# Performance work log

Hardware: AMD Instinct MI355X
Metric: run time of the kernel (lower is better)

Reference implementation:

```python
import jax, jax.numpy as jnp
import numpy as np

MAX_RADIUS = 4.0
N_BASIS = 10
MUL = 8                    # output_size -> '8x0e' multiplicity
OUT_MULS = (16, 8, 4)      # irreps_output = 16x0e + 8x1o + 4x2e
L_DIMS = (1, 3, 5)
N_NODES = 10000
N_EDGES = 131072
N_GRAPHS = 64
WEIGHT_NUMEL = MUL * MUL * sum(OUT_MULS)  # 1792


def _silu(x):
    return x * jax.nn.sigmoid(x)


def _sph_harm(u):
    # e3nn real spherical harmonics lmax=2, normalize=True, 'component' normalization
    x, y, z = u[:, 0], u[:, 1], u[:, 2]
    s3, s5, s15 = 3.0 ** 0.5, 5.0 ** 0.5, 15.0 ** 0.5
    sh0 = jnp.ones_like(x)[:, None]
    sh1 = jnp.stack([s3 * x, s3 * y, s3 * z], -1)
    sh2 = jnp.stack([s15 * x * z, s15 * x * y,
                     s5 * (y * y - 0.5 * (x * x + z * z)),
                     s15 * y * z, 0.5 * s15 * (z * z - x * x)], -1)
    return sh0, sh1, sh2


def _soft_one_hot(x):
    # e3nn soft_one_hot_linspace, basis='gaussian', cutoff=True
    values = jnp.linspace(0.0, MAX_RADIUS, N_BASIS + 2)[1:-1]
    step = MAX_RADIUS / (N_BASIS + 1)
    diff = (x[:, None] - values) / step
    return jnp.exp(-diff * diff) / 1.12


def setup_inputs() -> dict:
    key = jax.random.key(0)
    ks = jax.random.split(key, 16)
    return {
        "pos": jax.random.normal(ks[0], (N_NODES, 3), jnp.float32) * 2.0,
        "A": jax.random.randint(ks[1], (N_NODES,), 0, 10),
        "batch": jnp.sort(jax.random.randint(ks[2], (N_NODES,), 0, N_GRAPHS)),
        "edge_src": jax.random.randint(ks[3], (N_EDGES,), 0, N_NODES),
        "edge_dst": jax.random.randint(ks[4], (N_EDGES,), 0, N_NODES),
        "edge_shifts": jax.random.normal(ks[5], (N_EDGES, 3), jnp.float32) * 0.1,
        "cell": jax.random.normal(ks[6], (N_GRAPHS, 3, 3), jnp.float32),
        "embed_table": jax.random.normal(ks[7], (10, 16), jnp.float32),
        "fit_W1": jax.random.normal(ks[8], (16, 64), jnp.float32) * (2.0 / 16) ** 0.5,
        "fit_b1": jnp.zeros((64,), jnp.float32),
        "fit_W2": jax.random.normal(ks[9], (64, 32), jnp.float32) * (2.0 / 64) ** 0.5,
        "fit_b2": jnp.zeros((32,), jnp.float32),
        "fit_W3": jax.random.normal(ks[10], (32, MUL), jnp.float32) * (2.0 / 32) ** 0.5,
        "fit_b3": jnp.zeros((MUL,), jnp.float32),
        "fc_W1": jax.random.normal(ks[11], (N_BASIS, 64), jnp.float32),
        "fc_W2": jax.random.normal(ks[12], (64, 64), jnp.float32),
        "fc_W3": jax.random.normal(ks[13], (64, 64), jnp.float32),
        "fc_W4": jax.random.normal(ks[14], (64, WEIGHT_NUMEL), jnp.float32),
    }


def reference(pos, A, batch, edge_src, edge_dst, edge_shifts, cell,
              embed_table, fit_W1, fit_b1, fit_W2, fit_b2, fit_W3, fit_b3,
              fc_W1, fc_W2, fc_W3, fc_W4):
    # --- edge vectors with periodic shifts ---
    shift_vecs = jnp.einsum('ni,nij->nj', edge_shifts, cell[batch[edge_src]])
    edge_vec = pos[edge_dst] - pos[edge_src] + shift_vecs      # [E,3]
    edge_length = jnp.linalg.norm(edge_vec, axis=1)            # [E]
    unit = edge_vec / jnp.maximum(edge_length, 1e-9)[:, None]

    # --- per-node scalar features: embedding -> MLP (MainNet2) ---
    h = embed_table[A]
    h = _silu(h @ fit_W1 + fit_b1)
    h = _silu(h @ fit_W2 + fit_b2)
    Ai = h @ fit_W3 + fit_b3                                   # [N,8]

    sh0, sh1, sh2 = _sph_harm(unit)                            # [E,1],[E,3],[E,5]

    # --- radial MLP (e3nn FullyConnectedNet: silu, 1/sqrt(fan_in) weight scaling) ---
    emb = _soft_one_hot(edge_length) * (N_BASIS ** 0.5)
    w = _silu(emb @ fc_W1 / N_BASIS ** 0.5)
    w = _silu(w @ fc_W2 / 8.0)
    w = _silu(w @ fc_W3 / 8.0)
    w = w @ fc_W4 / 8.0                                        # [E,1792]

    Ai_src = Ai[edge_src]                                      # [E,8]
    Ai_dst = Ai[edge_dst]                                      # [E,8]

    # FullTensorProduct(8x0e, sh) is the outer product f_in[e,u,m] = Ai_src[e,u]*sh_l[e,m];
    # FullyConnectedTensorProduct with scalar irreps_in2 reduces per l-channel to a
    # weighted contraction with path normalization 1/sqrt(mul1*mul2) = 1/8.
    blocks, off = [], 0
    for mul_out, dim, sh_l in zip(OUT_MULS, L_DIMS, (sh0, sh1, sh2)):
        n = MUL * MUL * mul_out
        Wl = w[:, off:off + n].reshape(-1, MUL, MUL, mul_out)
        off += n
        blk = jnp.einsum('eu,em,ev,euvw->ewm', Ai_src, sh_l, Ai_dst, Wl) / MUL
        blocks.append(blk.reshape(-1, mul_out * dim))
    edge_features = jnp.concatenate(blocks, -1)                # [E,60]

    # --- scatter-mean aggregation to destination nodes ---
    n_nodes = pos.shape[0]
    counts = jax.ops.segment_sum(jnp.ones((edge_dst.shape[0],), jnp.float32),
                                 edge_dst, num_segments=n_nodes)
    out = jax.ops.segment_sum(edge_features, edge_dst, num_segments=n_nodes)
    return out / jnp.maximum(counts, 1.0)[:, None]             # [N,60]
```

## Files before the change

kernel.cpp:

```cpp
#include <hip/hip_runtime.h>
#include <hip/hip_bf16.h>
#include <math.h>

#define NN 10000
#define NE 131072

typedef __attribute__((ext_vector_type(8))) short short8;
typedef __attribute__((ext_vector_type(4))) float f32x4;

__device__ __forceinline__ float silu_f(float x) {
    return x / (1.0f + __expf(-x));
}

__device__ __forceinline__ unsigned short f2bf(float f) {
    unsigned int u = __float_as_uint(f);
    u += 0x7FFFu + ((u >> 16) & 1u);
    return (unsigned short)(u >> 16);
}

__device__ __forceinline__ unsigned int pk_bf16(float lo, float hi) {
    __hip_bfloat162 h = __float22bfloat162_rn(float2{lo, hi});
    return *reinterpret_cast<unsigned int*>(&h);
}

__global__ __launch_bounds__(256)
void prep_kernel(const int* __restrict__ A,
                 const int* __restrict__ edst,
                 const float* __restrict__ emb_tab,
                 const float* __restrict__ W1, const float* __restrict__ b1,
                 const float* __restrict__ W2, const float* __restrict__ b2,
                 const float* __restrict__ W3, const float* __restrict__ b3,
                 const float* __restrict__ fcW1,
                 const float* __restrict__ fcW2,
                 const float* __restrict__ fcW3,
                 const float* __restrict__ fcW4,
                 int* __restrict__ hist,
                 float* __restrict__ outg,
                 float* __restrict__ Ai,
                 unsigned short* __restrict__ Wg,
                 unsigned short* __restrict__ Bg)
{
    const int blk = blockIdx.x;
    const int tid = threadIdx.x;

    if (blk < 40) {
        int nd = blk * 256 + tid;
        if (nd >= NN) return;
        int a = A[nd];
        float h[16];
#pragma unroll
        for (int i = 0; i < 16; ++i) h[i] = emb_tab[a * 16 + i];
        float h1[64];
#pragma unroll
        for (int j = 0; j < 64; ++j) h1[j] = b1[j];
#pragma unroll
        for (int i = 0; i < 16; ++i) {
            float hv = h[i];
#pragma unroll
            for (int j = 0; j < 64; ++j) h1[j] += hv * W1[i * 64 + j];
        }
#pragma unroll
        for (int j = 0; j < 64; ++j) h1[j] = silu_f(h1[j]);
        float h2[32];
#pragma unroll
        for (int j = 0; j < 32; ++j) h2[j] = b2[j];
#pragma unroll
        for (int i = 0; i < 64; ++i) {
            float hv = h1[i];
#pragma unroll
            for (int j = 0; j < 32; ++j) h2[j] += hv * W2[i * 32 + j];
        }
#pragma unroll
        for (int j = 0; j < 32; ++j) h2[j] = silu_f(h2[j]);
#pragma unroll
        for (int j = 0; j < 8; ++j) {
            float s = b3[j];
#pragma unroll
            for (int i = 0; i < 32; ++i) s += h2[i] * W3[i * 8 + j];
            Ai[nd * 8 + j] = s;
        }
    } else if (blk < 80) {
        int i = (blk - 40) * 256 + tid;
        int j    = i & 7;
        int lane = (i >> 3) & 63;
        int f    = i >> 9;
        int q = lane >> 4, n = lane & 15;
        int L, kf, nt;
        if (f < 4)       { L = 1; kf = 0;             nt = f; }
        else if (f < 12) { L = 2; kf = (f - 4) >> 2;  nt = (f - 4) & 3; }
        else             { L = 3; kf = (f - 12) >> 2; nt = (f - 12) & 3; }
        int k = kf * 32 + q * 8 + j;
        int col = nt * 16 + n;
        float v = 0.0f;
        if (L == 1)      { if (k < 10) v = fcW1[k * 64 + col]; }
        else if (L == 2) v = fcW2[k * 64 + col];
        else             v = fcW3[k * 64 + col];
        Wg[i] = f2bf(v);
    } else if (blk < 592) {
        int i = (blk - 80) * 256 + tid;
        atomicAdd(&hist[edst[i]], 1);
        int j    = i & 7;
        int lane = (i >> 3) & 63;
        int nt   = (i >> 9) & 1;
        int h    = (i >> 10) & 1;
        int k    = i >> 11;
        int q = lane >> 4, n = lane & 15;
        int uv = h * 32 + q * 8 + j;
        int wc = nt * 16 + n;
        float v;
        if (wc < 16)      v = fcW4[k * 1792 + uv * 16 + wc];
        else if (wc < 24) v = fcW4[k * 1792 + 1024 + uv * 8 + (wc - 16)];
        else if (wc < 28) v = fcW4[k * 1792 + 1536 + uv * 4 + (wc - 24)];
        else              v = 0.0f;
        Bg[i] = f2bf(v);
    } else {
        int t = (blk - 592) * 256 + tid;
        float4 z = float4{0.f, 0.f, 0.f, 0.f};
        for (int r = t; r < 150000; r += 25600)
            ((float4*)outg)[r] = z;
    }
}

__global__ __launch_bounds__(256)
void scanrank_kernel(const int* __restrict__ edst,
                     const int* __restrict__ hist,
                     int* __restrict__ poscnt,
                     int* __restrict__ sortidx)
{
    __shared__ int offs[NN];
    __shared__ int part[256];
    const int tid = threadIdx.x;

    int loc[40];
    int s = 0;
    if (tid < 250) {
        const int4* h4 = (const int4*)(hist) + tid * 10;
#pragma unroll
        for (int v = 0; v < 10; ++v) {
            int4 x = h4[v];
            loc[v * 4 + 0] = x.x; loc[v * 4 + 1] = x.y;
            loc[v * 4 + 2] = x.z; loc[v * 4 + 3] = x.w;
            s += x.x + x.y + x.z + x.w;
        }
    } else {
#pragma unroll
        for (int r = 0; r < 40; ++r) loc[r] = 0;
    }
    part[tid] = s;
    __syncthreads();
#pragma unroll
    for (int off = 1; off < 256; off <<= 1) {
        int v = (tid >= off) ? part[tid - off] : 0;
        __syncthreads();
        part[tid] += v;
        __syncthreads();
    }
    if (tid < 250) {
        int run = part[tid] - s;
        int base = tid * 40;
#pragma unroll
        for (int r = 0; r < 40; ++r) { offs[base + r] = run; run += loc[r]; }
    }
    __syncthreads();

    int e = blockIdx.x * 256 + tid;
    int d = edst[e];
    int slot = offs[d] + atomicAdd(&poscnt[d], 1);
    sortidx[slot] = e;
}

__global__ __launch_bounds__(256, 2)
void edge_fused_kernel(const float* __restrict__ pos,
                       const int* __restrict__ batch,
                       const int* __restrict__ esrc,
                       const int* __restrict__ edst,
                       const float* __restrict__ shifts,
                       const float* __restrict__ cell,
                       const unsigned short* __restrict__ Wg,
                       const unsigned short* __restrict__ Bg,
                       const int* __restrict__ sortidx,
                       const float* __restrict__ Ai,
                       const int* __restrict__ hist,
                       float* __restrict__ out_g)
{
    __shared__ __align__(16) unsigned char  WBs[20480];
    __shared__ __align__(16) unsigned short actb[4][64 * 68];
    __shared__ int   sdb[256];
    __shared__ __align__(16) float shb[4][64 * 8];

    const int tid  = threadIdx.x;
    const int wave = tid >> 6;
    const int lane = tid & 63;
    const int q    = lane >> 4;
    const int n    = lane & 15;
    const int i    = blockIdx.x * 256 + wave * 64 + lane;

#pragma unroll
    for (int it = 0; it < 5; ++it) {
        int idx = it * 256 + tid;
        const unsigned short* gp = Wg + idx * 8;
        unsigned char* lb = WBs + (it * 256 + wave * 64) * 16;
        __builtin_amdgcn_global_load_lds(
            (const __attribute__((address_space(1))) unsigned int*)gp,
            (__attribute__((address_space(3))) unsigned int*)lb, 16, 0, 0);
    }

    unsigned short* actw = actb[wave];

    int e = sortidx[i];
    int s = esrc[e], d = edst[e];
    sdb[wave * 64 + lane] = s | (d << 16);
    int b = batch[s];
    const float* C = cell + b * 9;
    float sx = shifts[e * 3 + 0], sy = shifts[e * 3 + 1], sz = shifts[e * 3 + 2];
    float vx = pos[d * 3 + 0] - pos[s * 3 + 0] + sx * C[0] + sy * C[3] + sz * C[6];
    float vy = pos[d * 3 + 1] - pos[s * 3 + 1] + sx * C[1] + sy * C[4] + sz * C[7];
    float vz = pos[d * 3 + 2] - pos[s * 3 + 2] + sx * C[2] + sy * C[5] + sz * C[8];
    float len = sqrtf(vx * vx + vy * vy + vz * vz);
    float inv = 1.0f / fmaxf(len, 1e-9f);
    float ux = vx * inv, uy = vy * inv, uz = vz * inv;
    {
        const float s3c  = 1.7320508075688772f;
        const float s5c  = 2.2360679774997896f;
        const float s15c = 3.872983346207417f;
        float* shw = shb[wave];
        *(float4*)&shw[lane * 8]     = float4{s3c * ux, s3c * uy, s3c * uz,
                                              s15c * ux * uz};
        *(float4*)&shw[lane * 8 + 4] = float4{s15c * ux * uy,
                                              s5c * (uy * uy - 0.5f * (ux * ux + uz * uz)),
                                              s15c * uy * uz,
                                              0.5f * s15c * (uz * uz - ux * ux)};
    }

    float embv[10];
    float base = len * 2.75f;
#pragma unroll
    for (int ii = 0; ii < 10; ++ii) {
        float ddv = base - (float)(ii + 1);
        embv[ii] = __expf(-ddv * ddv) * (1.0f / 1.12f);
    }
    {
        unsigned int u0 = pk_bf16(embv[0], embv[1]);
        unsigned int u1 = pk_bf16(embv[2], embv[3]);
        unsigned int u2 = pk_bf16(embv[4], embv[5]);
        unsigned int u3 = pk_bf16(embv[6], embv[7]);
        unsigned int u4 = pk_bf16(embv[8], embv[9]);
        uint2* arow = (uint2*)&actw[lane * 68];
        arow[0] = uint2{u0, u1};
        arow[1] = uint2{u2, u3};
        arow[2] = uint2{u4, 0u};
        arow[3] = uint2{0u, 0u};
        arow[4] = uint2{0u, 0u};
        arow[5] = uint2{0u, 0u};
        arow[6] = uint2{0u, 0u};
        arow[7] = uint2{0u, 0u};
    }

    __syncthreads();

    union AF { unsigned int u[4]; short8 s8; };
    const f32x4 Z4 = (f32x4){0.f, 0.f, 0.f, 0.f};
    const unsigned short* Wbuf = (const unsigned short*)WBs;

    auto loadA = [&](int t, int kf) -> AF {
        const unsigned short* ap = &actw[(t * 16 + n) * 68 + kf * 32 + q * 8];
        uint2 a = *(const uint2*)ap;
        uint2 c = *(const uint2*)(ap + 4);
        AF f; f.u[0] = a.x; f.u[1] = a.y; f.u[2] = c.x; f.u[3] = c.y;
        return f;
    };
    auto loadW = [&](int f) -> short8 {
        return *(const short8*)&Wbuf[(f * 64 + lane) * 8];
    };

    {
        AF A1[4];
#pragma unroll
        for (int t = 0; t < 4; ++t) A1[t] = loadA(t, 0);
#pragma unroll
        for (int nt = 0; nt < 4; ++nt) {
            short8 W0 = loadW(nt);
            f32x4 Cc[4];
#pragma unroll
            for (int t = 0; t < 4; ++t)
                Cc[t] = __builtin_amdgcn_mfma_f32_16x16x32_bf16(A1[t].s8, W0, Z4, 0, 0, 0);
#pragma unroll
            for (int t = 0; t < 4; ++t)
#pragma unroll
                for (int r = 0; r < 4; ++r)
                    actw[(t * 16 + q * 4 + r) * 68 + nt * 16 + n] = f2bf(silu_f(Cc[t][r]));
        }
    }

    {
        AF A2[4][2];
#pragma unroll
        for (int t = 0; t < 4; ++t)
#pragma unroll
            for (int kf = 0; kf < 2; ++kf) A2[t][kf] = loadA(t, kf);
#pragma unroll
        for (int nt = 0; nt < 4; ++nt) {
            short8 Wk0 = loadW(4 + nt);
            short8 Wk1 = loadW(8 + nt);
            f32x4 Cc[4];
#pragma unroll
            for (int t = 0; t < 4; ++t) {
                Cc[t] = __builtin_amdgcn_mfma_f32_16x16x32_bf16(A2[t][0].s8, Wk0, Z4, 0, 0, 0);
                Cc[t] = __builtin_amdgcn_mfma_f32_16x16x32_bf16(A2[t][1].s8, Wk1, Cc[t], 0, 0, 0);
            }
#pragma unroll
            for (int t = 0; t < 4; ++t)
#pragma unroll
                for (int r = 0; r < 4; ++r)
                    actw[(t * 16 + q * 4 + r) * 68 + nt * 16 + n] = f2bf(silu_f(Cc[t][r] * 0.125f));
        }
    }

    {
        AF A3[4][2];
#pragma unroll
        for (int t = 0; t < 4; ++t)
#pragma unroll
            for (int kf = 0; kf < 2; ++kf) A3[t][kf] = loadA(t, kf);
#pragma unroll
        for (int nt = 0; nt < 4; ++nt) {
            short8 Wk0 = loadW(12 + nt);
            short8 Wk1 = loadW(16 + nt);
            f32x4 Cc[4];
#pragma unroll
            for (int t = 0; t < 4; ++t) {
                Cc[t] = __builtin_amdgcn_mfma_f32_16x16x32_bf16(A3[t][0].s8, Wk0, Z4, 0, 0, 0);
                Cc[t] = __builtin_amdgcn_mfma_f32_16x16x32_bf16(A3[t][1].s8, Wk1, Cc[t], 0, 0, 0);
            }
#pragma unroll
            for (int t = 0; t < 4; ++t)
#pragma unroll
                for (int r = 0; r < 4; ++r)
                    actw[(nt * 16 + n) * 68 + t * 16 + q * 4 + r] = f2bf(silu_f(Cc[t][r] * 0.125f));
        }
    }

    __syncthreads();

    auto stageB = [&](int c, int buf) {
#pragma unroll
        for (int it = 0; it < 2; ++it) {
            int idx = it * 256 + tid;
            const unsigned char* gp = ((const unsigned char*)Bg) + c * 8192 + idx * 16;
            unsigned char* lb = WBs + buf * 8192 + (it * 256 + wave * 64) * 16;
            __builtin_amdgcn_global_load_lds(
                (const __attribute__((address_space(1))) unsigned int*)gp,
                (__attribute__((address_space(3))) unsigned int*)lb, 16, 0, 0);
        }
    };
    stageB(0, 0);

    AF P[4][2];
#pragma unroll
    for (int t = 0; t < 4; ++t) {
        int eL = wave * 64 + t * 16 + n;
        int sd = sdb[eL];
        int ss  = sd & 0xFFFF;
        int dd2 = sd >> 16;
        float As0 = Ai[ss * 8 + q];
        float As1 = Ai[ss * 8 + 4 + q];
        float4 d0 = *(const float4*)&Ai[dd2 * 8];
        float4 d1 = *(const float4*)&Ai[dd2 * 8 + 4];
        float Ad[8] = {d0.x, d0.y, d0.z, d0.w, d1.x, d1.y, d1.z, d1.w};
#pragma unroll
        for (int h = 0; h < 2; ++h) {
            float s0 = h ? As1 : As0;
            P[t][h].u[0] = pk_bf16(s0 * Ad[0], s0 * Ad[1]);
            P[t][h].u[1] = pk_bf16(s0 * Ad[2], s0 * Ad[3]);
            P[t][h].u[2] = pk_bf16(s0 * Ad[4], s0 * Ad[5]);
            P[t][h].u[3] = pk_bf16(s0 * Ad[6], s0 * Ad[7]);
        }
    }

    f32x4 out[4][2];
#pragma unroll
    for (int t = 0; t < 4; ++t)
#pragma unroll
        for (int nt = 0; nt < 2; ++nt)
            out[t][nt] = (f32x4){0.f, 0.f, 0.f, 0.f};

    __syncthreads();

#pragma unroll 1
    for (int c = 0; c < 32; ++c) {
        int cur = c & 1;
        if (c < 31) stageB(c + 1, cur ^ 1);
#pragma unroll
        for (int kk = 0; kk < 2; ++kk) {
            int k = c * 2 + kk;
            short8 Bf[2][2];
#pragma unroll
            for (int h = 0; h < 2; ++h)
#pragma unroll
                for (int nt = 0; nt < 2; ++nt)
                    Bf[h][nt] = *(const short8*)(WBs + cur * 8192 +
                                 ((kk * 2 + h) * 2 + nt) * 1024 + lane * 16);
#pragma unroll
            for (int t = 0; t < 4; ++t) {
                uint2 v = *(const uint2*)&actw[k * 68 + t * 16 + q * 4];
                float w0 = __uint_as_float(v.x << 16);
                float w1 = __uint_as_float(v.x & 0xFFFF0000u);
                float w2 = __uint_as_float(v.y << 16);
                float w3 = __uint_as_float(v.y & 0xFFFF0000u);
#pragma unroll
                for (int nt = 0; nt < 2; ++nt) {
                    f32x4 Q = __builtin_amdgcn_mfma_f32_16x16x32_bf16(
                        P[t][0].s8, Bf[0][nt], Z4, 0, 0, 0);
                    Q = __builtin_amdgcn_mfma_f32_16x16x32_bf16(
                        P[t][1].s8, Bf[1][nt], Q, 0, 0, 0);
                    out[t][nt][0] += w0 * Q[0];
                    out[t][nt][1] += w1 * Q[1];
                    out[t][nt][2] += w2 * Q[2];
                    out[t][nt][3] += w3 * Q[3];
                }
            }
        }
        __syncthreads();
    }

    float* featL = (float*)actw;
#pragma unroll
    for (int t = 0; t < 4; ++t) {
#pragma unroll
        for (int r = 0; r < 4; ++r) {
            int row = t * 16 + q * 4 + r;
            featL[row * 33 + n]      = out[t][0][r];
            featL[row * 33 + 16 + n] = out[t][1][r];
        }
    }

    if (lane < 60) {
        int j = lane;
        int cc, sidx = 0;
        bool is0 = (j < 16);
        if (j < 16)      { cc = j; }
        else if (j < 40) { cc = 16 + (j - 16) / 3; sidx = (j - 16) % 3; }
        else             { cc = 24 + (j - 40) / 5; sidx = 3 + (j - 40) % 5; }

        const float* shw = shb[wave];
        int cur_d = sdb[wave * 64] >> 16;
        float acc = 0.f;
        for (int e2 = 0; e2 < 64; ++e2) {
            int d_e = sdb[wave * 64 + e2] >> 16;
            if (d_e != cur_d) {
                int cnt = hist[cur_d];
                atomicAdd(&out_g[cur_d * 60 + j], acc * (1.0f / 64.0f) / (float)cnt);
                acc = 0.f;
                cur_d = d_e;
            }
            float f  = featL[e2 * 33 + cc];
            float sh = shw[e2 * 8 + sidx];
            if (is0) sh = 1.0f;
            acc += f * sh;
        }
        int cnt = hist[cur_d];
        atomicAdd(&out_g[cur_d * 60 + j], acc * (1.0f / 64.0f) / (float)cnt);
    }
}

extern "C" void kernel_launch(void* const* d_in, const int* in_sizes, int n_in,
                              void* d_out, int out_size, void* d_ws, size_t ws_size,
                              hipStream_t stream)
{
    const float* pos     = (const float*)d_in[0];
    const int*   A       = (const int*)d_in[1];
    const int*   batch   = (const int*)d_in[2];
    const int*   esrc    = (const int*)d_in[3];
    const int*   edst    = (const int*)d_in[4];
    const float* shifts  = (const float*)d_in[5];
    const float* cell    = (const float*)d_in[6];
    const float* emb_tab = (const float*)d_in[7];
    const float* fitW1   = (const float*)d_in[8];
    const float* fitb1   = (const float*)d_in[9];
    const float* fitW2   = (const float*)d_in[10];
    const float* fitb2   = (const float*)d_in[11];
    const float* fitW3   = (const float*)d_in[12];
    const float* fitb3   = (const float*)d_in[13];
    const float* fcW1    = (const float*)d_in[14];
    const float* fcW2    = (const float*)d_in[15];
    const float* fcW3    = (const float*)d_in[16];
    const float* fcW4    = (const float*)d_in[17];

    float* out = (float*)d_out;

    char* W = (char*)d_ws;
    float* Ai      = (float*)W;  W += (size_t)NN * 8 * 4;
    int* sortidx   = (int*)W;    W += (size_t)NE * 4;
    int* hist      = (int*)W;    W += (size_t)NN * 4;
    int* poscnt    = (int*)W;    W += (size_t)NN * 4;
    unsigned short* Bg = (unsigned short*)W; W += (size_t)131072 * 2;
    unsigned short* Wg = (unsigned short*)W; W += (size_t)10240 * 2;

    hipMemsetAsync(hist, 0, (size_t)NN * 4 * 2, stream);

    prep_kernel<<<692, 256, 0, stream>>>(
        A, edst, emb_tab, fitW1, fitb1, fitW2, fitb2, fitW3, fitb3,
        fcW1, fcW2, fcW3, fcW4, hist, out, Ai, Wg, Bg);

    scanrank_kernel<<<NE / 256, 256, 0, stream>>>(edst, hist, poscnt, sortidx);

    edge_fused_kernel<<<NE / 256, 256, 0, stream>>>(
        pos, batch, esrc, edst, shifts, cell, Wg, Bg,
        sortidx, Ai, hist, out);
}
```

Baseline: 199.2 us.

## Fuse scan/rank into edge kernel via grid barrier; coalesce fcW4 repack reads

Merges the scan-and-rank kernel and the edge kernel into one launch. The two phases share a single 64.5 KB LDS buffer and are separated by a software grid-wide barrier built on an atomic counter, which is zeroed in the workspace memset. The fcW4-to-bf16 repack in the prep kernel now walks the source linearly and scatters into the tiled layout, so reads are coalesced, and it zero-fills the padding columns separately. The aim is to remove one kernel launch and its drain gap. The cost is a spin barrier that assumes all 512 blocks are co-resident, and the kernel hangs if they are not.

```diff
diff --git a/kernel.cpp b/kernel.cpp
--- a/kernel.cpp
+++ b/kernel.cpp
@@ -97,22 +97,34 @@
         else             v = fcW3[k * 64 + col];
         Wg[i] = f2bf(v);
     } else if (blk < 592) {
-        int i = (blk - 80) * 256 + tid;
-        atomicAdd(&hist[edst[i]], 1);
-        int j    = i & 7;
-        int lane = (i >> 3) & 63;
-        int nt   = (i >> 9) & 1;
-        int h    = (i >> 10) & 1;
-        int k    = i >> 11;
-        int q = lane >> 4, n = lane & 15;
-        int uv = h * 32 + q * 8 + j;
-        int wc = nt * 16 + n;
-        float v;
-        if (wc < 16)      v = fcW4[k * 1792 + uv * 16 + wc];
-        else if (wc < 24) v = fcW4[k * 1792 + 1024 + uv * 8 + (wc - 16)];
-        else if (wc < 28) v = fcW4[k * 1792 + 1536 + uv * 4 + (wc - 24)];
-        else              v = 0.0f;
-        Bg[i] = f2bf(v);
+        int linear = (blk - 80) * 256 + tid;
+        atomicAdd(&hist[edst[linear]], 1);
+        if (linear < 114688) {
+            int k = linear / 1792;
+            int t = linear - k * 1792;
+            int uv, wc;
+            if (t < 1024)      { uv = t >> 4;            wc = t & 15; }
+            else if (t < 1536) { int r = t - 1024; uv = r >> 3; wc = 16 + (r & 7); }
+            else               { int r = t - 1536; uv = r >> 2; wc = 24 + (r & 3); }
+            int h  = uv >> 5;
+            int q  = (uv >> 3) & 3;
+            int j  = uv & 7;
+            int nt = wc >> 4;
+            int n  = wc & 15;
+            int i  = (k << 11) | (h << 10) | (nt << 9) | (((q << 4) | n) << 3) | j;
+            Bg[i] = f2bf(fcW4[linear]);
+        } else {
+            int z  = linear - 114688;
+            int k  = z >> 8;
+            int r  = z & 255;
+            int uv = r >> 2;
+            int c2 = z & 3;
+            int h  = uv >> 5;
+            int q  = (uv >> 3) & 3;
+            int j  = uv & 7;
+            int i  = (k << 11) | (h << 10) | (1 << 9) | (((q << 4) | (12 + c2)) << 3) | j;
+            Bg[i] = 0;
+        }
     } else {
         int t = (blk - 592) * 256 + tid;
         float4 z = float4{0.f, 0.f, 0.f, 0.f};
@@ -121,74 +133,87 @@
     }
 }
 
-__global__ __launch_bounds__(256)
-void scanrank_kernel(const int* __restrict__ edst,
-                     const int* __restrict__ hist,
-                     int* __restrict__ poscnt,
-                     int* __restrict__ sortidx)
+__global__ __launch_bounds__(256, 2)
+void scanrank_edge_kernel(const float* __restrict__ pos,
+                          const int* __restrict__ batch,
+                          const int* __restrict__ esrc,
+                          const int* __restrict__ edst,
+                          const float* __restrict__ shifts,
+                          const float* __restrict__ cell,
+                          const unsigned short* __restrict__ Wg,
+                          const unsigned short* __restrict__ Bg,
+                          const float* __restrict__ Ai,
+                          const int* __restrict__ hist,
+                          int* __restrict__ poscnt,
+                          int* __restrict__ sortidx,
+                          int* __restrict__ bar,
+                          float* __restrict__ out_g)
 {
-    __shared__ int offs[NN];
-    __shared__ int part[256];
+    __shared__ __align__(16) unsigned char SM[64512];
+
     const int tid = threadIdx.x;
 
-    int loc[40];
-    int s = 0;
-    if (tid < 250) {
-        const int4* h4 = (const int4*)(hist) + tid * 10;
-#pragma unroll
-        for (int v = 0; v < 10; ++v) {
-            int4 x = h4[v];
-            loc[v * 4 + 0] = x.x; loc[v * 4 + 1] = x.y;
-            loc[v * 4 + 2] = x.z; loc[v * 4 + 3] = x.w;
-            s += x.x + x.y + x.z + x.w;
-        }
-    } else {
-#pragma unroll
-        for (int r = 0; r < 40; ++r) loc[r] = 0;
-    }
-    part[tid] = s;
+    {
+        int* offs = (int*)SM;
+        int* part = (int*)(SM + 40000);
+
+        int loc[40];
+        int s = 0;
+        if (tid < 250) {
+            const int4* h4 = (const int4*)(hist) + tid * 10;
+#pragma unroll
+            for (int v = 0; v < 10; ++v) {
+                int4 x = h4[v];
+                loc[v * 4 + 0] = x.x; loc[v * 4 + 1] = x.y;
+                loc[v * 4 + 2] = x.z; loc[v * 4 + 3] = x.w;
+                s += x.x + x.y + x.z + x.w;
+            }
+        } else {
+#pragma unroll
+            for (int r = 0; r < 40; ++r) loc[r] = 0;
+        }
+        part[tid] = s;
+        __syncthreads();
+#pragma unroll
+        for (int off = 1; off < 256; off <<= 1) {
+            int v = (tid >= off) ? part[tid - off] : 0;
+            __syncthreads();
+            part[tid] += v;
+            __syncthreads();
+        }
+        if (tid < 250) {
+            int run = part[tid] - s;
+            int base = tid * 40;
+#pragma unroll
+            for (int r = 0; r < 40; ++r) { offs[base + r] = run; run += loc[r]; }
+        }
+        __syncthreads();
+
+        int e = blockIdx.x * 256 + tid;
+        int d = edst[e];
+        int slot = offs[d] + atomicAdd(&poscnt[d], 1);
+        sortidx[slot] = e;
+    }
+
     __syncthreads();
-#pragma unroll
-    for (int off = 1; off < 256; off <<= 1) {
-        int v = (tid >= off) ? part[tid - off] : 0;
-        __syncthreads();
-        part[tid] += v;
-        __syncthreads();
-    }
-    if (tid < 250) {
-        int run = part[tid] - s;
-        int base = tid * 40;
-#pragma unroll
-        for (int r = 0; r < 40; ++r) { offs[base + r] = run; run += loc[r]; }
+    if (tid == 0) {
+        __threadfence();
+        __hip_atomic_fetch_add(bar, 1, __ATOMIC_RELAXED,
+                               __HIP_MEMORY_SCOPE_AGENT);
+        while (__hip_atomic_load(bar, __ATOMIC_RELAXED,
+                                 __HIP_MEMORY_SCOPE_AGENT) < (int)gridDim.x)
+            __builtin_amdgcn_s_sleep(2);
+        __threadfence();
     }
     __syncthreads();
 
-    int e = blockIdx.x * 256 + tid;
-    int d = edst[e];
-    int slot = offs[d] + atomicAdd(&poscnt[d], 1);
-    sortidx[slot] = e;
-}
-
-__global__ __launch_bounds__(256, 2)
-void edge_fused_kernel(const float* __restrict__ pos,
-                       const int* __restrict__ batch,
-                       const int* __restrict__ esrc,
-                       const int* __restrict__ edst,
-                       const float* __restrict__ shifts,
-                       const float* __restrict__ cell,
-                       const unsigned short* __restrict__ Wg,
-                       const unsigned short* __restrict__ Bg,
-                       const int* __restrict__ sortidx,
-                       const float* __restrict__ Ai,
-                       const int* __restrict__ hist,
-                       float* __restrict__ out_g)
-{
-    __shared__ __align__(16) unsigned char  WBs[20480];
-    __shared__ __align__(16) unsigned short actb[4][64 * 68];
-    __shared__ int   sdb[256];
-    __shared__ __align__(16) float shb[4][64 * 8];
-
-    const int tid  = threadIdx.x;
+    unsigned char* WBs = SM;
+    unsigned short (*actb)[64 * 68] =
+        (unsigned short (*)[64 * 68])(SM + 20480);
+    int*   sdb = (int*)(SM + 20480 + 34816);
+    float (*shb)[64 * 8] =
+        (float (*)[64 * 8])(SM + 20480 + 34816 + 1024);
+
     const int wave = tid >> 6;
     const int lane = tid & 63;
     const int q    = lane >> 4;
@@ -207,7 +232,8 @@
 
     unsigned short* actw = actb[wave];
 
-    int e = sortidx[i];
+    int e = __hip_atomic_load(&sortidx[i], __ATOMIC_RELAXED,
+                              __HIP_MEMORY_SCOPE_AGENT);
     int s = esrc[e], d = edst[e];
     sdb[wave * 64 + lane] = s | (d << 16);
     int b = batch[s];
@@ -493,18 +519,17 @@
     int* sortidx   = (int*)W;    W += (size_t)NE * 4;
     int* hist      = (int*)W;    W += (size_t)NN * 4;
     int* poscnt    = (int*)W;    W += (size_t)NN * 4;
+    int* bar       = (int*)W;    W += 16;
     unsigned short* Bg = (unsigned short*)W; W += (size_t)131072 * 2;
     unsigned short* Wg = (unsigned short*)W; W += (size_t)10240 * 2;
 
-    hipMemsetAsync(hist, 0, (size_t)NN * 4 * 2, stream);
+    hipMemsetAsync(hist, 0, (size_t)NN * 4 * 2 + 16, stream);
 
     prep_kernel<<<692, 256, 0, stream>>>(
         A, edst, emb_tab, fitW1, fitb1, fitW2, fitb2, fitW3, fitb3,
         fcW1, fcW2, fcW3, fcW4, hist, out, Ai, Wg, Bg);
 
-    scanrank_kernel<<<NE / 256, 256, 0, stream>>>(edst, hist, poscnt, sortidx);
-
-    edge_fused_kernel<<<NE / 256, 256, 0, stream>>>(
+    scanrank_edge_kernel<<<NE / 256, 256, 0, stream>>>(
         pos, batch, esrc, edst, shifts, cell, Wg, Bg,
-        sortidx, Ai, hist, out);
+        Ai, hist, poscnt, sortidx, bar, out);
 }
```

After: 249.9 us. 25.5% more time.
